# Optimization experiments

Measured on AMD Instinct MI355X. Metric: run time of the kernel, lower is better.

The kernel has to match this reference:

```python
import jax, jax.numpy as jnp
import numpy as np

B, S, D, H = 4, 2048, 1024, 16
DK = D // H


def setup_inputs() -> dict:
    key = jax.random.key(0)
    ks = jax.random.split(key, 16)
    s = 0.02
    inp = {
        "Q": jax.random.normal(ks[0], (B, S, D), jnp.float32),
        "K": jax.random.normal(ks[1], (B, S, D), jnp.float32),
        "V": jax.random.normal(ks[2], (B, S, D), jnp.float32),
        "mask": jax.random.randint(ks[3], (B, 1, S, S), 0, 2, jnp.int32),
        "wq": jax.random.normal(ks[4], (D, D), jnp.float32) * s,
        "bq": jnp.zeros((D,), jnp.float32),
        "wk": jax.random.normal(ks[5], (D, D), jnp.float32) * s,
        "bk": jnp.zeros((D,), jnp.float32),
        "wv": jax.random.normal(ks[6], (D, D), jnp.float32) * s,
        "bv": jnp.zeros((D,), jnp.float32),
        "wo": jax.random.normal(ks[7], (D, D), jnp.float32) * s,
        "bo": jnp.zeros((D,), jnp.float32),
        "na_q_w": jax.random.normal(ks[8], (DK, DK), jnp.float32) * 0.1,
        "na_q_b": jnp.zeros((DK,), jnp.float32),
        "na_k_w": jax.random.normal(ks[9], (DK, DK), jnp.float32) * 0.1,
        "na_k_b": jnp.zeros((DK,), jnp.float32),
        "temperature": jnp.ones((H, 1, 1), jnp.float32),
        "rms_w": jnp.ones((D,), jnp.float32),
    }
    return inp


def _split_heads(x):
    # [B,S,D] -> [B,H,S,DK]
    return x.reshape(B, S, H, DK).transpose(0, 2, 1, 3)


def reference(Q, K, V, mask, wq, bq, wk, bk, wv, bv, wo, bo,
              na_q_w, na_q_b, na_k_w, na_k_b, temperature, rms_w):
    q = _split_heads(Q @ wq.T + bq)
    k = _split_heads(K @ wk.T + bk)
    v = _split_heads(V @ wv.T + bv)
    # NeuralAttention: tanh-transformed Q,K then scaled dot product
    qn = jnp.tanh(q @ na_q_w.T + na_q_b)
    kn = jnp.tanh(k @ na_k_w.T + na_k_b)
    scores = jnp.einsum("bhqd,bhkd->bhqk", qn, kn) / (DK ** 0.5)
    scores = scores / temperature  # [H,1,1] broadcasts over [B,H,S,S]
    scores = jnp.where(mask == 0, jnp.float32(-1e9), scores)
    attn = jax.nn.softmax(scores, axis=-1)
    ctx = jnp.einsum("bhqk,bhkd->bhqd", attn, v)
    out = ctx.transpose(0, 2, 1, 3).reshape(B, S, D) @ wo.T + bo
    # RMSNorm
    out = out * jax.lax.rsqrt(jnp.mean(out * out, axis=-1, keepdims=True) + 1e-8) * rms_w
    return out
```

## Files before the change

### kernel.cpp

```cpp
#include <hip/hip_runtime.h>
#include <hip/hip_bf16.h>

constexpr int Bc  = 4;
constexpr int Sc  = 2048;
constexpr int Dc  = 1024;
constexpr int Hc  = 16;
constexpr int DKc = 64;
constexpr int Mc  = Bc * Sc;

typedef __bf16 bf16x8 __attribute__((ext_vector_type(8)));
typedef float  f32x4  __attribute__((ext_vector_type(4)));
typedef unsigned short ushort_t;

#define DEV __device__ __forceinline__

DEV unsigned short f2bf(float f) {
    unsigned u = __builtin_bit_cast(unsigned, f);
    u += 0x7FFFu + ((u >> 16) & 1u);
    return (unsigned short)(u >> 16);
}
DEV unsigned pack2(float a, float b) {
    return (unsigned)f2bf(a) | ((unsigned)f2bf(b) << 16);
}
DEV void gl16(const void* g, void* l) {
    __builtin_amdgcn_global_load_lds((const __attribute__((address_space(1))) unsigned int*)g,
                                     (__attribute__((address_space(3))) unsigned int*)l, 16, 0, 0);
}
DEV f32x4 mfma16(bf16x8 a, bf16x8 b, f32x4 c) {
    return __builtin_amdgcn_mfma_f32_16x16x32_bf16(a, b, c, 0, 0, 0);
}
DEV unsigned spread4(unsigned x) {
    x = (x | (x << 12)) & 0x000F000Fu;
    x = (x | (x << 6))  & 0x03030303u;
    x = (x | (x << 3))  & 0x11111111u;
    return x;
}


__global__ __launch_bounds__(256) void fold_w2(const float* __restrict__ naqw,
                                               const float* __restrict__ wq,
                                               unsigned short* __restrict__ wqf,
                                               const float* __restrict__ nakw,
                                               const float* __restrict__ wk,
                                               unsigned short* __restrict__ wkf,
                                               const float* __restrict__ bq,
                                               const float* __restrict__ naqb,
                                               float* __restrict__ bqf,
                                               const float* __restrict__ bk,
                                               const float* __restrict__ nakb,
                                               float* __restrict__ bkf) {
    const int colg = blockIdx.x, h = blockIdx.y, z = blockIdx.z;
    if (z == 2) {
        if (h >= 2) return;
        const float* na = h ? nakw : naqw;
        const float* b  = h ? bk : bq;
        const float* nb = h ? nakb : naqb;
        float* out      = h ? bkf : bqf;
        int idx = colg * 256 + threadIdx.x;
        if (idx >= Dc) return;
        int hh = idx >> 6, i = idx & 63;
        float acc = nb[i];
        for (int t = 0; t < DKc; ++t) acc += na[i * DKc + t] * b[hh * DKc + t];
        out[idx] = acc;
        return;
    }
    const float* na = z ? nakw : naqw;
    const float* w  = z ? wk : wq;
    unsigned short* out = z ? wkf : wqf;
    const int col = colg * 256 + threadIdx.x;

    __shared__ float nal[64 * 64];
    for (int i = threadIdx.x; i < 4096; i += 256) nal[i] = na[i];

    float wr[64];
#pragma unroll
    for (int t = 0; t < 64; ++t) wr[t] = w[(h * 64 + t) * Dc + col];
    __syncthreads();

    for (int i = 0; i < 64; ++i) {
        float acc = 0.f;
#pragma unroll
        for (int t = 0; t < 64; ++t) acc += nal[i * 64 + t] * wr[t];
        out[(h * 64 + i) * Dc + col] = f2bf(acc);
    }
}

constexpr int CONVB = (3 * Mc * Dc + 2 * Dc * Dc) / 8 / 256;
constexpr int MASKB = Bc * Sc * Sc / 1024;
__global__ __launch_bounds__(256) void conv_mask(const float* __restrict__ Q,
                                                 const float* __restrict__ K,
                                                 const float* __restrict__ V,
                                                 const float* __restrict__ wv,
                                                 const float* __restrict__ wo,
                                                 ushort_t* __restrict__ qb,
                                                 ushort_t* __restrict__ kb,
                                                 ushort_t* __restrict__ vb,
                                                 ushort_t* __restrict__ wvf,
                                                 ushort_t* __restrict__ wof,
                                                 const int* __restrict__ m,
                                                 unsigned* __restrict__ mbits) {
    const int bid = blockIdx.x;
    const int tid = threadIdx.x;
    if (bid < CONVB) {
        size_t i = ((size_t)bid * 256 + tid) * 8;
        constexpr size_t N = (size_t)Mc * Dc;
        constexpr size_t W = (size_t)Dc * Dc;
        const float* src; ushort_t* dst; size_t off;
        if      (i < N)         { src = Q;  dst = qb;  off = i; }
        else if (i < 2 * N)     { src = K;  dst = kb;  off = i - N; }
        else if (i < 3 * N)     { src = V;  dst = vb;  off = i - 2 * N; }
        else if (i < 3 * N + W) { src = wv; dst = wvf; off = i - 3 * N; }
        else                    { src = wo; dst = wof; off = i - 3 * N - W; }
        float4 a = *(const float4*)(src + off), b = *(const float4*)(src + off + 4);
        uint4 o;
        o.x = pack2(a.x, a.y); o.y = pack2(a.z, a.w);
        o.z = pack2(b.x, b.y); o.w = pack2(b.z, b.w);
        *(uint4*)(dst + off) = o;
    } else {
        const int mb = bid - CONVB;
        const size_t p0 = ((size_t)mb * 256 + tid) * 4;
        const int ing = (int)(p0 & 63);
        const int nat = (((ing >> 4) & 1) << 5) | (((ing >> 2) & 3) << 3)
                      | (((ing >> 5) & 1) << 2);
        const int4 mv = *(const int4*)(m + ((p0 & ~(size_t)63) | (size_t)nat));
        unsigned nib = (unsigned)(mv.x != 0) | ((unsigned)(mv.y != 0) << 1)
                     | ((unsigned)(mv.z != 0) << 2) | ((unsigned)(mv.w != 0) << 3);
        unsigned long long bal0 = __ballot((nib & 1u) != 0);
        unsigned long long bal1 = __ballot((nib & 2u) != 0);
        unsigned long long bal2 = __ballot((nib & 4u) != 0);
        unsigned long long bal3 = __ballot((nib & 8u) != 0);
        const int lane = tid & 63, s = tid >> 6;
        const int sh8 = (lane & 7) * 8;
        unsigned bb0 = (unsigned)(bal0 >> sh8) & 0xFFu;
        unsigned bb1 = (unsigned)(bal1 >> sh8) & 0xFFu;
        unsigned bb2 = (unsigned)(bal2 >> sh8) & 0xFFu;
        unsigned bb3 = (unsigned)(bal3 >> sh8) & 0xFFu;
        unsigned word = spread4(bb0) | (spread4(bb1) << 1)
                      | (spread4(bb2) << 2) | (spread4(bb3) << 3);
        if (lane < 8) mbits[(size_t)mb * 32 + s * 8 + lane] = word;
    }
}

template <int EPI, int SWZ>
__global__ __launch_bounds__(256) void gemm_bt(const ushort_t* __restrict__ A,
                                               const ushort_t* __restrict__ B,
                                               const float* __restrict__ bias,
                                               void* __restrict__ outp,
                                               int Mdim, int Ndim, int Kdim) {
    __shared__ __align__(16) unsigned char As[2][16384];
    __shared__ __align__(16) unsigned char Bs[2][16384];

    int bx = blockIdx.x, by = blockIdx.y;
    {
        int nwg = gridDim.x * gridDim.y;
        int L = by * gridDim.x + bx;
        int cpx = nwg >> 3;
        int orig = (L & 7) * cpx + (L >> 3);
        if constexpr (SWZ == 1) { bx = orig % gridDim.x; by = orig / gridDim.x; }
        else                    { by = orig % gridDim.y; bx = orig / gridDim.y; }
    }

    const int tid = threadIdx.x, lane = tid & 63, wave = tid >> 6;
    const int wr = wave >> 1, wc = wave & 1;
    const int q = lane & 15, g = lane >> 4;
    const int m0 = by * 128, n0 = bx * 128;

    const int strow = lane >> 3, stcol = (lane & 7) * 8;
    const ushort_t* Ab = A + (size_t)(m0 + strow) * Kdim + stcol;
    const ushort_t* Bb = B + (size_t)(n0 + strow) * Kdim + stcol;

    f32x4 acc[4][4] = {};
    const int nK = Kdim >> 6;

#pragma unroll
    for (int i = 0; i < 4; ++i) {
        const int ro = (wave * 4 + i) * 8;
        gl16(Ab + (size_t)ro * Kdim, As[0] + (wave * 4 + i) * 1024);
        gl16(Bb + (size_t)ro * Kdim, Bs[0] + (wave * 4 + i) * 1024);
    }
    __syncthreads();

    for (int kt = 0; kt < nK; ++kt) {
        const int cur = kt & 1;
        if (kt + 1 < nK) {
            const int k1 = (kt + 1) << 6;
#pragma unroll
            for (int i = 0; i < 4; ++i) {
                const int ro = (wave * 4 + i) * 8;
                gl16(Ab + (size_t)ro * Kdim + k1, As[cur ^ 1] + (wave * 4 + i) * 1024);
                gl16(Bb + (size_t)ro * Kdim + k1, Bs[cur ^ 1] + (wave * 4 + i) * 1024);
            }
        }
#pragma unroll
        for (int s = 0; s < 2; ++s) {
            const int cb = s * 64 + g * 16;
            bf16x8 a[4], b[4];
#pragma unroll
            for (int m = 0; m < 4; ++m)
                a[m] = *(const bf16x8*)(As[cur] + (wr * 64 + m * 16 + q) * 128 + cb);
#pragma unroll
            for (int n = 0; n < 4; ++n)
                b[n] = *(const bf16x8*)(Bs[cur] + (wc * 64 + n * 16 + q) * 128 + cb);
#pragma unroll
            for (int m = 0; m < 4; ++m)
#pragma unroll
                for (int n = 0; n < 4; ++n)
                    acc[m][n] = mfma16(a[m], b[n], acc[m][n]);
        }
        __syncthreads();
    }

#pragma unroll
    for (int m = 0; m < 4; ++m)
#pragma unroll
        for (int n = 0; n < 4; ++n) {
            int gn = n0 + wc * 64 + n * 16 + q;
#pragma unroll
            for (int r = 0; r < 4; ++r) {
                int gm = m0 + wr * 64 + m * 16 + (g << 2) + r;
                float v = acc[m][n][r];
                if constexpr (EPI == 1) {
                    v += bias[gm];
                    int hh = gm >> 6, dk = gm & 63, b = gn >> 11, s = gn & 2047;
                    int kt2 = s >> 7, kloc = s & 127;
                    int eofs = ((kloc * 2) ^ ((dk & 7) << 4)) >> 1;
                    size_t idx = ((size_t)(b * Hc + hh)) * Sc * DKc + (size_t)kt2 * 8192 + dk * 128 + eofs;
                    ((unsigned short*)outp)[idx] = f2bf(v);
                } else {
                    v += bias[gn];
                    ((float*)outp)[(size_t)gm * Ndim + gn] = v;
                }
            }
        }
}

__global__ __launch_bounds__(512, 2) void gemm_qk256(const ushort_t* __restrict__ qb,
                                                     const ushort_t* __restrict__ wqf,
                                                     const float* __restrict__ bqf,
                                                     ushort_t* __restrict__ qnb,
                                                     const ushort_t* __restrict__ kb,
                                                     const ushort_t* __restrict__ wkf,
                                                     const float* __restrict__ bkf,
                                                     ushort_t* __restrict__ knb,
                                                     const float* __restrict__ temp) {
    __shared__ __align__(16) unsigned char As[2][32768];
    __shared__ __align__(16) unsigned char Bs[2][32768];

    const int zz = blockIdx.z;
    const ushort_t* A = zz ? kb : qb;
    const ushort_t* B = zz ? wkf : wqf;
    const float* bias = zz ? bkf : bqf;

    int L = blockIdx.y * gridDim.x + blockIdx.x;
    int orig = (L & 7) * 16 + (L >> 3);
    int bx = orig & 3, by = orig >> 2;

    const int tid = threadIdx.x, lane = tid & 63, wave = tid >> 6;
    const int wr = wave >> 2, wc = wave & 3;
    const int q = lane & 15, g = lane >> 4;
    const int m0 = by * 256, n0 = bx * 256;

    const int strow = lane >> 3, stcol = (lane & 7) * 8;
    const ushort_t* Ab = A + (size_t)(m0 + strow) * Dc + stcol;
    const ushort_t* Bb = B + (size_t)(n0 + strow) * Dc + stcol;

    f32x4 acc[8][4] = {};
    constexpr int nK = Dc >> 6;

#define STAGE256(buf, k0)                                                       \
    {                                                                           \
        _Pragma("unroll")                                                       \
        for (int i = 0; i < 4; ++i) {                                           \
            const int j = wave * 4 + i;                                         \
            gl16(Ab + (size_t)(j * 8) * Dc + (k0), As[buf] + j * 1024);         \
            gl16(Bb + (size_t)(j * 8) * Dc + (k0), Bs[buf] + j * 1024);         \
        }                                                                       \
    }

    STAGE256(0, 0);
    __syncthreads();

    for (int kt = 0; kt < nK; ++kt) {
        const int cur = kt & 1;
        if (kt + 1 < nK) STAGE256(cur ^ 1, (kt + 1) << 6);
#pragma unroll
        for (int s = 0; s < 2; ++s) {
            const int cb = s * 64 + g * 16;
            bf16x8 a[8], b[4];
#pragma unroll
            for (int m = 0; m < 8; ++m)
                a[m] = *(const bf16x8*)(As[cur] + (wr * 128 + m * 16 + q) * 128 + cb);
#pragma unroll
            for (int n = 0; n < 4; ++n)
                b[n] = *(const bf16x8*)(Bs[cur] + (wc * 64 + n * 16 + q) * 128 + cb);
#pragma unroll
            for (int m = 0; m < 8; ++m)
#pragma unroll
                for (int n = 0; n < 4; ++n)
                    acc[m][n] = mfma16(a[m], b[n], acc[m][n]);
        }
        __syncthreads();
    }
#undef STAGE256

#pragma unroll
    for (int m = 0; m < 8; ++m)
#pragma unroll
        for (int n = 0; n < 4; ++n) {
            int gn = n0 + wc * 64 + n * 16 + q;
            float sc_h = 1.f;
            if (zz == 0) sc_h = 0.18033688011112042f * __builtin_amdgcn_rcpf(temp[gn >> 6]);
#pragma unroll
            for (int r = 0; r < 4; ++r) {
                int gm = m0 + wr * 128 + m * 16 + (g << 2) + r;
                float v = tanhf(acc[m][n][r] + bias[gn]);
                int b = gm >> 11, s = gm & 2047, hh = gn >> 6, dk = gn & 63;
                if (zz == 0) {
                    qnb[(((size_t)(b * Hc + hh)) * Sc + s) * DKc + dk] = f2bf(v * sc_h);
                } else {
                    int kt2 = s >> 7, nr = s & 127;
                    int prow = (nr & 64) | (((nr >> 5) & 1) << 4) | (((nr >> 3) & 3) << 2)
                             | (((nr >> 2) & 1) << 5) | (nr & 3);
                    int eofs = ((dk * 2) ^ ((prow & 7) << 4)) >> 1;
                    size_t idx = ((size_t)(b * Hc + hh)) * Sc * DKc + (size_t)kt2 * 8192 + prow * 64 + eofs;
                    knb[idx] = f2bf(v);
                }
            }
        }
}

__global__ __launch_bounds__(512, 2) void attn_k(const ushort_t* __restrict__ qn,
                                                 const ushort_t* __restrict__ kn,
                                                 const ushort_t* __restrict__ vtp,
                                                 const unsigned* __restrict__ mbits,
                                                 ushort_t* __restrict__ ctxb) {
    __shared__ __align__(16) unsigned char Kl[2][16384];
    __shared__ __align__(16) unsigned char Vl[2][16384];

    const int tid = threadIdx.x, lane = tid & 63, wave = tid >> 6;
    const int q = lane & 15, g = lane >> 4;

    const int wg = blockIdx.x;
    const int orig = (wg & 7) * 64 + (wg >> 3);
    const int qt = orig & 7, h = (orig >> 3) & 15, b = orig >> 7;
    const int q0 = qt * 256;
    const int qr0 = q0 + wave * 32 + q;
    const size_t headoff = ((size_t)(b * Hc + h)) * Sc * DKc;

    const unsigned char* Ksrc = (const unsigned char*)(kn + headoff);
    const unsigned char* Vsrc = (const unsigned char*)(vtp + headoff);
    const int so = wave * 1024 + lane * 16;
    const int ld = wave * 1024;

    bf16x8 qf[2][2];
    {
        const ushort_t* p0 = qn + headoff + (size_t)qr0 * DKc + g * 8;
        qf[0][0] = *(const bf16x8*)p0;
        qf[0][1] = *(const bf16x8*)(p0 + 32);
        qf[1][0] = *(const bf16x8*)(p0 + 16 * DKc);
        qf[1][1] = *(const bf16x8*)(p0 + 16 * DKc + 32);
    }
    const unsigned* mr0 = mbits + ((size_t)b * Sc + qr0) * (Sc / 32);
    const unsigned* mr1 = mr0 + 16 * (Sc / 32);

    bf16x8 ones;
#pragma unroll
    for (int i = 0; i < 8; ++i) ones[i] = (__bf16)1.0f;

    f32x4 ctxa[2][4] = {};
    f32x4 lacc[2] = {};
    const int swz = (q & 7) << 4;
    const int sh = g << 2;

    gl16(Ksrc + so,        &Kl[0][ld]);
    gl16(Ksrc + 8192 + so, &Kl[0][8192 + ld]);
    gl16(Vsrc + so,        &Vl[0][ld]);
    gl16(Vsrc + 8192 + so, &Vl[0][8192 + ld]);
    __syncthreads();

    for (int kt = 0; kt < Sc / 128; ++kt) {
        const int cur = kt & 1;
        if (kt < Sc / 128 - 1) {
            const unsigned char* ks = Ksrc + (kt + 1) * 16384;
            const unsigned char* vs = Vsrc + (kt + 1) * 16384;
            gl16(ks + so,        &Kl[cur ^ 1][ld]);
            gl16(ks + 8192 + so, &Kl[cur ^ 1][8192 + ld]);
            gl16(vs + so,        &Vl[cur ^ 1][ld]);
            gl16(vs + 8192 + so, &Vl[cur ^ 1][8192 + ld]);
        }
        unsigned mwq[2][4];
        {
            uint4 t0 = *(const uint4*)(mr0 + kt * 4);
            uint4 t1 = *(const uint4*)(mr1 + kt * 4);
            mwq[0][0] = t0.x >> sh; mwq[0][1] = t0.y >> sh;
            mwq[0][2] = t0.z >> sh; mwq[0][3] = t0.w >> sh;
            mwq[1][0] = t1.x >> sh; mwq[1][1] = t1.y >> sh;
            mwq[1][2] = t1.z >> sh; mwq[1][3] = t1.w >> sh;
        }
        const unsigned char* Kb = Kl[cur];
        const unsigned char* Vb = Vl[cur];

#pragma unroll
        for (int kh = 0; kh < 2; ++kh) {
            f32x4 s0[4] = {}, s1[4] = {};
            __builtin_amdgcn_s_setprio(1);
#pragma unroll
            for (int f = 0; f < 4; ++f) {
                const int ro = (kh * 64 + f * 16 + q) * 128;
                bf16x8 a0 = *(const bf16x8*)(Kb + ro + ((g * 16) ^ swz));
                bf16x8 a1 = *(const bf16x8*)(Kb + ro + ((64 + g * 16) ^ swz));
                s0[f] = mfma16(a0, qf[0][0], s0[f]);
                s0[f] = mfma16(a1, qf[0][1], s0[f]);
                s1[f] = mfma16(a0, qf[1][0], s1[f]);
                s1[f] = mfma16(a1, qf[1][1], s1[f]);
            }
            __builtin_amdgcn_s_setprio(0);

#pragma unroll
            for (int f = 0; f < 4; ++f) {
                unsigned w0 = mwq[0][kh * 2 + (f >> 1)];
                unsigned w1 = mwq[1][kh * 2 + (f >> 1)];
#pragma unroll
                for (int r = 0; r < 4; ++r) {
                    const unsigned bitc = 1u << (((f & 1) << 4) + r);
                    float v0 = (w0 & bitc) ? s0[f][r] : -1e30f;
                    float v1 = (w1 & bitc) ? s1[f][r] : -1e30f;
                    s0[f][r] = __builtin_amdgcn_exp2f(v0);
                    s1[f][r] = __builtin_amdgcn_exp2f(v1);
                }
            }

            bf16x8 pa0[2], pa1[2];
#pragma unroll
            for (int cs = 0; cs < 2; ++cs)
#pragma unroll
                for (int r = 0; r < 4; ++r) {
                    pa0[cs][r]     = (__bf16)s0[cs][r];
                    pa0[cs][4 + r] = (__bf16)s0[cs + 2][r];
                    pa1[cs][r]     = (__bf16)s1[cs][r];
                    pa1[cs][4 + r] = (__bf16)s1[cs + 2][r];
                }

            __builtin_amdgcn_s_setprio(1);
#pragma unroll
            for (int cs = 0; cs < 2; ++cs) {
                const int csg = kh * 2 + cs;
                lacc[0] = mfma16(pa0[cs], ones, lacc[0]);
                lacc[1] = mfma16(pa1[cs], ones, lacc[1]);
#pragma unroll
                for (int j = 0; j < 4; ++j) {
                    bf16x8 vb = *(const bf16x8*)(Vb + (j * 16 + q) * 256 + ((csg * 64 + g * 16) ^ swz));
                    ctxa[0][j] = mfma16(pa0[cs], vb, ctxa[0][j]);
                    ctxa[1][j] = mfma16(pa1[cs], vb, ctxa[1][j]);
                }
            }
            __builtin_amdgcn_s_setprio(0);
        }
        __syncthreads();
    }

#pragma unroll
    for (int qg = 0; qg < 2; ++qg) {
        f32x4 linv;
#pragma unroll
        for (int r = 0; r < 4; ++r) linv[r] = __builtin_amdgcn_rcpf(lacc[qg][r]);
#pragma unroll
        for (int j = 0; j < 4; ++j)
#pragma unroll
            for (int r = 0; r < 4; ++r) {
                int srow = q0 + wave * 32 + qg * 16 + (g << 2) + r;
                int col = h * DKc + j * 16 + q;
                float v = ctxa[qg][j][r] * linv[r];
                ctxb[((size_t)b * Sc + srow) * Dc + col] = __builtin_bit_cast(unsigned short, (__bf16)v);
            }
    }
}

__global__ __launch_bounds__(256) void rmsnorm_k(float* __restrict__ out,
                                                 const float* __restrict__ w) {
    const int row = blockIdx.x, tid = threadIdx.x;
    float4* p = (float4*)(out + (size_t)row * Dc) + tid;
    float4 v = *p;
    float ss = v.x * v.x + v.y * v.y + v.z * v.z + v.w * v.w;
#pragma unroll
    for (int o = 32; o >= 1; o >>= 1) ss += __shfl_xor(ss, o);
    __shared__ float sm[4];
    if ((tid & 63) == 0) sm[tid >> 6] = ss;
    __syncthreads();
    float tot = sm[0] + sm[1] + sm[2] + sm[3];
    float r = rsqrtf(tot * (1.f / Dc) + 1e-8f);
    float4 wv = *((const float4*)w + tid);
    v.x *= r * wv.x; v.y *= r * wv.y; v.z *= r * wv.z; v.w *= r * wv.w;
    *p = v;
}

extern "C" void kernel_launch(void* const* d_in, const int* in_sizes, int n_in,
                              void* d_out, int out_size, void* d_ws, size_t ws_size,
                              hipStream_t stream) {
    (void)in_sizes; (void)n_in; (void)out_size; (void)ws_size;
    const float* Q    = (const float*)d_in[0];
    const float* K    = (const float*)d_in[1];
    const float* V    = (const float*)d_in[2];
    const int*   mask = (const int*)  d_in[3];
    const float* wq   = (const float*)d_in[4];
    const float* bq   = (const float*)d_in[5];
    const float* wk   = (const float*)d_in[6];
    const float* bk   = (const float*)d_in[7];
    const float* wv   = (const float*)d_in[8];
    const float* bv   = (const float*)d_in[9];
    const float* wo   = (const float*)d_in[10];
    const float* bo   = (const float*)d_in[11];
    const float* naqw = (const float*)d_in[12];
    const float* naqb = (const float*)d_in[13];
    const float* nakw = (const float*)d_in[14];
    const float* nakb = (const float*)d_in[15];
    const float* temp = (const float*)d_in[16];
    const float* rmsw = (const float*)d_in[17];

    char* ws = (char*)d_ws;
    size_t off = 0;
    auto take = [&](size_t n) { char* p = ws + off; off += (n + 255) & ~(size_t)255; return p; };
    unsigned short* vtb  = (unsigned short*)take((size_t)Mc * Dc * 2);
    unsigned short* qb   = (unsigned short*)take((size_t)Mc * Dc * 2);
    unsigned short* kb   = (unsigned short*)take((size_t)Mc * Dc * 2);
    unsigned short* vb   = (unsigned short*)take((size_t)Mc * Dc * 2);
    unsigned short* qnb  = (unsigned short*)take((size_t)Mc * Dc * 2);
    unsigned short* knb  = (unsigned short*)take((size_t)Mc * Dc * 2);
    unsigned short* wqf  = (unsigned short*)take((size_t)Dc * Dc * 2);
    unsigned short* wkf  = (unsigned short*)take((size_t)Dc * Dc * 2);
    unsigned short* wvf  = (unsigned short*)take((size_t)Dc * Dc * 2);
    unsigned short* wof  = (unsigned short*)take((size_t)Dc * Dc * 2);
    float*    bqf   = (float*)take(Dc * 4);
    float*    bkf   = (float*)take(Dc * 4);
    unsigned* mbits = (unsigned*)take((size_t)Bc * Sc * (Sc / 32) * 4);
    unsigned short* ctxb = kb;

    fold_w2<<<dim3(4, 16, 3), 256, 0, stream>>>(naqw, wq, wqf, nakw, wk, wkf,
                                                bq, naqb, bqf, bk, nakb, bkf);
    conv_mask<<<dim3(CONVB + MASKB), 256, 0, stream>>>(Q, K, V, wv, wo,
                                                       qb, kb, vb, wvf, wof,
                                                       mask, mbits);

    gemm_bt<1, 2><<<dim3(Mc / 128, Dc / 128), 256, 0, stream>>>(
        wvf, vb, bv, vtb, Dc, Mc, Dc);
    gemm_qk256<<<dim3(4, 32, 2), 512, 0, stream>>>(
        qb, wqf, bqf, qnb, kb, wkf, bkf, knb, temp);

    attn_k<<<dim3(512), 512, 0, stream>>>(qnb, knb, vtb, mbits, ctxb);

    gemm_bt<2, 1><<<dim3(Dc / 128, Mc / 128), 256, 0, stream>>>(
        ctxb, wof, bo, d_out, Mc, Dc, Dc);
    rmsnorm_k<<<dim3(Mc), 256, 0, stream>>>((float*)d_out, rmsw);
}
```

Measured before the change: 289.1 us.

## Swizzle LDS GEMM tiles and use partial vmcnt waits for deeper prefetch overlap

Both bf16 GEMM kernels now XOR-swizzle the 16-byte column chunk by row, on the global-to-LDS staging and on the LDS fragment reads, to cut LDS bank conflicts. The full __syncthreads after each stage is replaced by an explicit s_waitcnt vmcnt(8) and a raw s_barrier. This lets the next tile's loads stay in flight while only the current tile's loads are awaited. The risk is correctness of the hand-written wait counts, which assume exactly 8 outstanding loads per thread.

```diff
diff --git a/kernel.cpp b/kernel.cpp
--- a/kernel.cpp
+++ b/kernel.cpp
@@ -29,6 +29,8 @@
 DEV f32x4 mfma16(bf16x8 a, bf16x8 b, f32x4 c) {
     return __builtin_amdgcn_mfma_f32_16x16x32_bf16(a, b, c, 0, 0, 0);
 }
+DEV void wait_vm8() { asm volatile("s_waitcnt vmcnt(8)" ::: "memory"); __builtin_amdgcn_sched_barrier(0); }
+DEV void wait_vm0() { asm volatile("s_waitcnt vmcnt(0)" ::: "memory"); __builtin_amdgcn_sched_barrier(0); }
 DEV unsigned spread4(unsigned x) {
     x = (x | (x << 12)) & 0x000F000Fu;
     x = (x | (x << 6))  & 0x03030303u;
@@ -165,50 +167,51 @@
     const int q = lane & 15, g = lane >> 4;
     const int m0 = by * 128, n0 = bx * 128;
 
-    const int strow = lane >> 3, stcol = (lane & 7) * 8;
+    const int strow = lane >> 3;
+    const int stcol = (((lane & 7) ^ strow) * 8);
     const ushort_t* Ab = A + (size_t)(m0 + strow) * Kdim + stcol;
     const ushort_t* Bb = B + (size_t)(n0 + strow) * Kdim + stcol;
+    const int rswz = (q & 7) << 4;
 
     f32x4 acc[4][4] = {};
     const int nK = Kdim >> 6;
 
-#pragma unroll
-    for (int i = 0; i < 4; ++i) {
-        const int ro = (wave * 4 + i) * 8;
-        gl16(Ab + (size_t)ro * Kdim, As[0] + (wave * 4 + i) * 1024);
-        gl16(Bb + (size_t)ro * Kdim, Bs[0] + (wave * 4 + i) * 1024);
-    }
-    __syncthreads();
+#define STAGE(buf, k0)                                                          \
+    {                                                                           \
+        _Pragma("unroll")                                                       \
+        for (int i = 0; i < 4; ++i) {                                           \
+            const int ro = (wave * 4 + i) * 8;                                  \
+            gl16(Ab + (size_t)ro * Kdim + (k0), As[buf] + (wave * 4 + i) * 1024); \
+            gl16(Bb + (size_t)ro * Kdim + (k0), Bs[buf] + (wave * 4 + i) * 1024); \
+        }                                                                       \
+    }
+
+    STAGE(0, 0);
 
     for (int kt = 0; kt < nK; ++kt) {
         const int cur = kt & 1;
-        if (kt + 1 < nK) {
-            const int k1 = (kt + 1) << 6;
-#pragma unroll
-            for (int i = 0; i < 4; ++i) {
-                const int ro = (wave * 4 + i) * 8;
-                gl16(Ab + (size_t)ro * Kdim + k1, As[cur ^ 1] + (wave * 4 + i) * 1024);
-                gl16(Bb + (size_t)ro * Kdim + k1, Bs[cur ^ 1] + (wave * 4 + i) * 1024);
-            }
-        }
+        if (kt + 1 < nK) { STAGE(cur ^ 1, (kt + 1) << 6); wait_vm8(); }
+        else             { wait_vm0(); }
+        __builtin_amdgcn_s_barrier();
 #pragma unroll
         for (int s = 0; s < 2; ++s) {
             const int cb = s * 64 + g * 16;
             bf16x8 a[4], b[4];
 #pragma unroll
             for (int m = 0; m < 4; ++m)
-                a[m] = *(const bf16x8*)(As[cur] + (wr * 64 + m * 16 + q) * 128 + cb);
+                a[m] = *(const bf16x8*)(As[cur] + (wr * 64 + m * 16 + q) * 128 + (cb ^ rswz));
 #pragma unroll
             for (int n = 0; n < 4; ++n)
-                b[n] = *(const bf16x8*)(Bs[cur] + (wc * 64 + n * 16 + q) * 128 + cb);
+                b[n] = *(const bf16x8*)(Bs[cur] + (wc * 64 + n * 16 + q) * 128 + (cb ^ rswz));
 #pragma unroll
             for (int m = 0; m < 4; ++m)
 #pragma unroll
                 for (int n = 0; n < 4; ++n)
                     acc[m][n] = mfma16(a[m], b[n], acc[m][n]);
         }
-        __syncthreads();
-    }
+        __builtin_amdgcn_s_barrier();
+    }
+#undef STAGE
 
 #pragma unroll
     for (int m = 0; m < 4; ++m)
@@ -260,9 +263,11 @@
     const int q = lane & 15, g = lane >> 4;
     const int m0 = by * 256, n0 = bx * 256;
 
-    const int strow = lane >> 3, stcol = (lane & 7) * 8;
+    const int strow = lane >> 3;
+    const int stcol = (((lane & 7) ^ strow) * 8);
     const ushort_t* Ab = A + (size_t)(m0 + strow) * Dc + stcol;
     const ushort_t* Bb = B + (size_t)(n0 + strow) * Dc + stcol;
+    const int rswz = (q & 7) << 4;
 
     f32x4 acc[8][4] = {};
     constexpr int nK = Dc >> 6;
@@ -278,28 +283,29 @@
     }
 
     STAGE256(0, 0);
-    __syncthreads();
 
     for (int kt = 0; kt < nK; ++kt) {
         const int cur = kt & 1;
-        if (kt + 1 < nK) STAGE256(cur ^ 1, (kt + 1) << 6);
+        if (kt + 1 < nK) { STAGE256(cur ^ 1, (kt + 1) << 6); wait_vm8(); }
+        else             { wait_vm0(); }
+        __builtin_amdgcn_s_barrier();
 #pragma unroll
         for (int s = 0; s < 2; ++s) {
             const int cb = s * 64 + g * 16;
             bf16x8 a[8], b[4];
 #pragma unroll
             for (int m = 0; m < 8; ++m)
-                a[m] = *(const bf16x8*)(As[cur] + (wr * 128 + m * 16 + q) * 128 + cb);
+                a[m] = *(const bf16x8*)(As[cur] + (wr * 128 + m * 16 + q) * 128 + (cb ^ rswz));
 #pragma unroll
             for (int n = 0; n < 4; ++n)
-                b[n] = *(const bf16x8*)(Bs[cur] + (wc * 64 + n * 16 + q) * 128 + cb);
+                b[n] = *(const bf16x8*)(Bs[cur] + (wc * 64 + n * 16 + q) * 128 + (cb ^ rswz));
 #pragma unroll
             for (int m = 0; m < 8; ++m)
 #pragma unroll
                 for (int n = 0; n < 4; ++n)
                     acc[m][n] = mfma16(a[m], b[n], acc[m][n]);
         }
-        __syncthreads();
+        __builtin_amdgcn_s_barrier();
     }
 #undef STAGE256
 
```

After: 258.6 us. 10.5% less time.
